# Performance work log

Hardware: AMD Instinct MI355X
Metric: run time of the kernel (lower is better)

Reference implementation:

```python
import jax, jax.numpy as jnp
import numpy as np

N = 4000                      # number of Gaussians
VOL = (256, 256, 256)         # volume shape
W = 32                        # fixed local window size (covers max 3-sigma box)
SIG_LO, SIG_HI = 0.008, 0.018 # normalized-coordinate sigma range


def setup_inputs() -> dict:
    key = jax.random.key(0)
    k1, k2, k3 = jax.random.split(key, 3)
    centers = jax.random.uniform(k1, (N, 3), dtype=jnp.float32)            # normalized in [0,1]
    sigmas = SIG_LO + (SIG_HI - SIG_LO) * jax.random.uniform(k2, (N,), dtype=jnp.float32)
    intensities = jax.random.uniform(k3, (N,), dtype=jnp.float32)
    return {"centers": centers, "sigmas": sigmas, "intensities": intensities}


def reference(centers, sigmas, intensities):
    shape = jnp.array(VOL, dtype=jnp.int32)                 # (3,)
    scale = (shape - 1).astype(jnp.float32)                 # volume_shape - 1, as in torch

    center = centers * scale                                # (N,3) voxel coords
    cutoff = 3.0 * sigmas[:, None] * scale                  # (N,3)

    # Bounding box: min_idx = int(max(center-cutoff, 0)), max (exclusive) = min(int(min(center+cutoff, scale))+1, dim)
    min_f = jnp.maximum(center - cutoff, 0.0)
    max_f = jnp.minimum(center + cutoff, scale)
    min_i = jnp.floor(min_f).astype(jnp.int32)              # (N,3) inclusive
    max_i = jnp.minimum(jnp.floor(max_f).astype(jnp.int32) + 1, shape)  # (N,3) exclusive

    # Fixed-size window fully inside the volume; mask voxels outside the true bbox.
    start = jnp.clip(min_i, 0, shape - W)                   # (N,3)
    offs = jnp.arange(W, dtype=jnp.int32)
    idx = start[:, :, None] + offs                          # (N,3,W) voxel indices per axis
    valid = (idx >= min_i[:, :, None]) & (idx < max_i[:, :, None])  # (N,3,W)

    # Per-axis squared distance in normalized coords (grid = idx/(dim-1)).
    pos = idx.astype(jnp.float32) / scale[None, :, None]    # (N,3,W)
    d2 = (pos - centers[:, :, None]) ** 2                   # (N,3,W)
    dist2 = (d2[:, 0, :, None, None] + d2[:, 1, None, :, None] + d2[:, 2, None, None, :])  # (N,W,W,W)

    inv2s2 = 0.5 / (sigmas ** 2)                            # (N,)
    contrib = intensities[:, None, None, None] * jnp.exp(-dist2 * inv2s2[:, None, None, None])
    mask = (valid[:, 0, :, None, None] & valid[:, 1, None, :, None] & valid[:, 2, None, None, :])
    contrib = jnp.where(mask, contrib, 0.0)                 # (N,W,W,W)

    # Overlapping scatter-add into the flattened volume.
    lin = (idx[:, 0, :, None, None] * (VOL[1] * VOL[2])
           + idx[:, 1, None, :, None] * VOL[2]
           + idx[:, 2, None, None, :])                      # (N,W,W,W) int32
    vol = jnp.zeros(VOL[0] * VOL[1] * VOL[2], dtype=jnp.float32)
    vol = vol.at[lin.reshape(-1)].add(contrib.reshape(-1))
    return vol.reshape(VOL)
```

## Files before the change

kernel.cpp:

```cpp
#include <hip/hip_runtime.h>

#define VOLD 256
#define CXD 16
#define CYD 16
#define CZD 32
#define NCELLS 2048
#define CAP 80

typedef float nfloat4 __attribute__((ext_vector_type(4)));
typedef float f2 __attribute__((ext_vector_type(2)));

__global__ __launch_bounds__(256) void splat_kernel(
    const float* __restrict__ centers, const float* __restrict__ sigmas,
    const float* __restrict__ intens, float* __restrict__ vol, int N)
{
    const int cell = blockIdx.x;
    const int czc = cell & 7;
    const int cyc = (cell >> 3) & 15;
    const int cxc = cell >> 7;
    const int vx0 = cxc * CXD, vy0 = cyc * CYD, vz0 = czc * CZD;
    const int t = threadIdx.x;

    __shared__ int           lcnt;
    __shared__ float4        pc4[CAP];
    __shared__ float         pint[CAP];
    __shared__ float         wx[CAP][CXD];
    __shared__ float         wy[CAP][CYD];
    __shared__ float         wz[CAP][CZD];
    __shared__ unsigned char wlist[4][CAP];

    if (t == 0) lcnt = 0;
    __syncthreads();

    const float axh = (float)(vx0 + CXD) + 0.5f, axl = (float)vx0 - 0.5f;
    const float ayh = (float)(vy0 + CYD) + 0.5f, ayl = (float)vy0 - 0.5f;
    const float azh = (float)(vz0 + CZD) + 0.5f, azl = (float)vz0 - 0.5f;

    const float4* c4 = (const float4*)centers;
    const float4* s4 = (const float4*)sigmas;
    const int npack = N >> 2;
    for (int i = t; i < npack; i += 256) {
        const float4 f0  = c4[3 * i];
        const float4 f1  = c4[3 * i + 1];
        const float4 f2v = c4[3 * i + 2];
        const float4 sg4 = s4[i];
        const float gx[4] = {f0.x, f0.w, f1.z, f2v.y};
        const float gy[4] = {f0.y, f1.x, f1.w, f2v.z};
        const float gz[4] = {f0.z, f1.y, f2v.x, f2v.w};
        const float gs[4] = {sg4.x, sg4.y, sg4.z, sg4.w};
        #pragma unroll
        for (int u = 0; u < 4; ++u) {
            const float m1 = fmaxf(fmaxf(fmaf(gx[u], 255.0f, -axh),
                                         fmaf(gy[u], 255.0f, -ayh)),
                                         fmaf(gz[u], 255.0f, -azh));
            const float m2 = fmaxf(fmaxf(fmaf(-gx[u], 255.0f, axl),
                                         fmaf(-gy[u], 255.0f, ayl)),
                                         fmaf(-gz[u], 255.0f, azl));
            if (fmaxf(m1, m2) < gs[u] * 765.0f) {
                const int p = atomicAdd(&lcnt, 1);
                if (p < CAP) {
                    pc4[p]  = make_float4(gx[u], gy[u], gz[u], gs[u]);
                    pint[p] = intens[4 * i + u];
                }
            }
        }
    }
    for (int g = (npack << 2) + t; g < N; g += 256) {
        const float cx = centers[3 * g], cy = centers[3 * g + 1], cz = centers[3 * g + 2];
        const float sg = sigmas[g];
        const float m1 = fmaxf(fmaxf(fmaf(cx, 255.0f, -axh), fmaf(cy, 255.0f, -ayh)),
                               fmaf(cz, 255.0f, -azh));
        const float m2 = fmaxf(fmaxf(fmaf(-cx, 255.0f, axl), fmaf(-cy, 255.0f, ayl)),
                               fmaf(-cz, 255.0f, azl));
        if (fmaxf(m1, m2) < sg * 765.0f) {
            const int p = atomicAdd(&lcnt, 1);
            if (p < CAP) { pc4[p] = make_float4(cx, cy, cz, sg); pint[p] = intens[g]; }
        }
    }
    __syncthreads();
    const int K = min(lcnt, CAP);

    for (int i = t; i < K * CXD; i += 256) {
        const int g = i >> 4, o = i & 15;
        const float4 p = pc4[g];
        const float cn = p.x, sig = p.w;
        const float cv = cn * 255.0f, cut = 3.0f * sig * 255.0f;
        const float fi = (float)(vx0 + o);
        float wv = 0.0f;
        if ((fi + 1.0f > cv - cut) && (fi <= fminf(cv + cut, 255.0f))) {
            const float d = fi * (1.0f / 255.0f) - cn;
            wv = __expf(-d * d * (0.5f / (sig * sig))) * pint[g];
        }
        wx[g][o] = wv;
    }
    for (int i = t; i < K * CYD; i += 256) {
        const int g = i >> 4, o = i & 15;
        const float4 p = pc4[g];
        const float cn = p.y, sig = p.w;
        const float cv = cn * 255.0f, cut = 3.0f * sig * 255.0f;
        const float fi = (float)(vy0 + o);
        float wv = 0.0f;
        if ((fi + 1.0f > cv - cut) && (fi <= fminf(cv + cut, 255.0f))) {
            const float d = fi * (1.0f / 255.0f) - cn;
            wv = __expf(-d * d * (0.5f / (sig * sig)));
        }
        wy[g][o] = wv;
    }
    for (int i = t; i < K * CZD; i += 256) {
        const int g = i >> 5, o = i & 31;
        const float4 p = pc4[g];
        const float cn = p.z, sig = p.w;
        const float cv = cn * 255.0f, cut = 3.0f * sig * 255.0f;
        const float fi = (float)(vz0 + o);
        float wv = 0.0f;
        if ((fi + 1.0f > cv - cut) && (fi <= fminf(cv + cut, 255.0f))) {
            const float d = fi * (1.0f / 255.0f) - cn;
            wv = __expf(-d * d * (0.5f / (sig * sig)));
        }
        wz[g][o] = wv;
    }
    __syncthreads();

    const int wv_id = t >> 6;
    const int lane  = t & 63;
    const float xw0 = (float)(vx0 + 8 * (wv_id & 1));
    const float yw0 = (float)(vy0 + 8 * (wv_id >> 1));

    int Kw = 0;
    for (int j0 = 0; j0 < K; j0 += 64) {
        const int j = j0 + lane;
        bool rel = false;
        if (j < K) {
            const float4 p = pc4[j];
            const float cvx = p.x * 255.0f, cvy = p.y * 255.0f;
            const float cut = p.w * 765.0f;
            rel = (cvx + cut >= xw0 - 1.0f) && (cvx - cut <= xw0 + 9.0f) &&
                  (cvy + cut >= yw0 - 1.0f) && (cvy - cut <= yw0 + 9.0f);
        }
        const unsigned long long m = __ballot(rel);
        if (rel) {
            const int pos = Kw + __popcll(m & ((1ull << lane) - 1ull));
            wlist[wv_id][pos] = (unsigned char)j;
        }
        Kw += __popcll(m);
    }

    const int zq = t & 7;
    const int xi = (t >> 3) & 15;
    const int yh = t >> 7;

    f2 acc[8][2];
    #pragma unroll
    for (int i = 0; i < 8; ++i) { acc[i][0] = 0.0f; acc[i][1] = 0.0f; }

    if (Kw > 0) {
        const unsigned char* wl = wlist[wv_id];
        const int kd0 = wl[0];
        const int kd1 = wl[(Kw > 1) ? 1 : 0];
        int kI2 = wl[(Kw > 2) ? 2 : (Kw - 1)];

        float4 ya0 = *(const float4*)&wy[kd0][8 * yh];
        float4 yb0 = *(const float4*)&wy[kd0][8 * yh + 4];
        float4 z0  = *(const float4*)&wz[kd0][4 * zq];
        float  x0v = wx[kd0][xi];
        float4 ya1 = *(const float4*)&wy[kd1][8 * yh];
        float4 yb1 = *(const float4*)&wy[kd1][8 * yh + 4];
        float4 z1  = *(const float4*)&wz[kd1][4 * zq];
        float  x1v = wx[kd1][xi];

        #pragma unroll 2
        for (int j = 0; j < Kw; ++j) {
            const int kI3 = wl[(j + 3 < Kw) ? (j + 3) : (Kw - 1)];
            const float4 ya2 = *(const float4*)&wy[kI2][8 * yh];
            const float4 yb2 = *(const float4*)&wy[kI2][8 * yh + 4];
            const float4 z2  = *(const float4*)&wz[kI2][4 * zq];
            const float  x2v = wx[kI2][xi];

            const f2 cz0 = {z0.x, z0.y};
            const f2 cz1 = {z0.z, z0.w};
            const float p0 = ya0.x * x0v, p1 = ya0.y * x0v;
            const float p2 = ya0.z * x0v, p3 = ya0.w * x0v;
            const float p4 = yb0.x * x0v, p5 = yb0.y * x0v;
            const float p6 = yb0.z * x0v, p7 = yb0.w * x0v;
            acc[0][0] += p0 * cz0; acc[0][1] += p0 * cz1;
            acc[1][0] += p1 * cz0; acc[1][1] += p1 * cz1;
            acc[2][0] += p2 * cz0; acc[2][1] += p2 * cz1;
            acc[3][0] += p3 * cz0; acc[3][1] += p3 * cz1;
            acc[4][0] += p4 * cz0; acc[4][1] += p4 * cz1;
            acc[5][0] += p5 * cz0; acc[5][1] += p5 * cz1;
            acc[6][0] += p6 * cz0; acc[6][1] += p6 * cz1;
            acc[7][0] += p7 * cz0; acc[7][1] += p7 * cz1;

            ya0 = ya1; yb0 = yb1; z0 = z1; x0v = x1v;
            ya1 = ya2; yb1 = yb2; z1 = z2; x1v = x2v;
            kI2 = kI3;
        }
    }

    #pragma unroll
    for (int yy = 0; yy < 8; ++yy) {
        const int y = 8 * yh + yy;
        const size_t lin = (size_t)(vx0 + xi) * (VOLD * VOLD)
                         + (size_t)(vy0 + y) * VOLD + (size_t)(vz0 + 4 * zq);
        nfloat4 v;
        v.x = acc[yy][0].x; v.y = acc[yy][0].y;
        v.z = acc[yy][1].x; v.w = acc[yy][1].y;
        __builtin_nontemporal_store(v, (nfloat4*)&vol[lin]);
    }
}

extern "C" void kernel_launch(void* const* d_in, const int* in_sizes, int n_in,
                              void* d_out, int out_size, void* d_ws, size_t ws_size,
                              hipStream_t stream) {
    const float* centers = (const float*)d_in[0];
    const float* sigmas  = (const float*)d_in[1];
    const float* intens  = (const float*)d_in[2];
    float* vol = (float*)d_out;
    const int N = in_sizes[1];

    splat_kernel<<<NCELLS, 256, 0, stream>>>(centers, sigmas, intens, vol, N);
}
```

Measured before the change: 25.57 us.

## Process two cells per block and replace syncthreads with lgkm-only barriers

Halves the grid to 1024 blocks, each looping over two cells (blockIdx and blockIdx+1024), with a per-cell counter so the shared counter needs no reset barrier. __syncthreads is replaced by a custom barrier that waits only on LDS/scalar counters, not global memory, so the nontemporal stores of the first cell need not drain before the second cell starts. The aim is to cut launch/tail overhead and overlap global stores with the next cell's culling. The cost is less parallelism across the GPU's CUs and serial per-block work.

```diff
diff --git a/kernel.cpp b/kernel.cpp
--- a/kernel.cpp
+++ b/kernel.cpp
@@ -4,24 +4,26 @@
 #define CXD 16
 #define CYD 16
 #define CZD 32
-#define NCELLS 2048
+#define NBLK 1024
 #define CAP 80
 
 typedef float nfloat4 __attribute__((ext_vector_type(4)));
 typedef float f2 __attribute__((ext_vector_type(2)));
+
+#define LGKM_BAR() do {                                     \
+    asm volatile("s_waitcnt lgkmcnt(0)" ::: "memory");      \
+    __builtin_amdgcn_sched_barrier(0);                      \
+    __builtin_amdgcn_s_barrier();                           \
+    __builtin_amdgcn_sched_barrier(0);                      \
+  } while (0)
 
 __global__ __launch_bounds__(256) void splat_kernel(
     const float* __restrict__ centers, const float* __restrict__ sigmas,
     const float* __restrict__ intens, float* __restrict__ vol, int N)
 {
-    const int cell = blockIdx.x;
-    const int czc = cell & 7;
-    const int cyc = (cell >> 3) & 15;
-    const int cxc = cell >> 7;
-    const int vx0 = cxc * CXD, vy0 = cyc * CYD, vz0 = czc * CZD;
     const int t = threadIdx.x;
 
-    __shared__ int           lcnt;
+    __shared__ int           lcnt[2];
     __shared__ float4        pc4[CAP];
     __shared__ float         pint[CAP];
     __shared__ float         wx[CAP][CXD];
@@ -29,183 +31,194 @@
     __shared__ float         wz[CAP][CZD];
     __shared__ unsigned char wlist[4][CAP];
 
-    if (t == 0) lcnt = 0;
-    __syncthreads();
-
-    const float axh = (float)(vx0 + CXD) + 0.5f, axl = (float)vx0 - 0.5f;
-    const float ayh = (float)(vy0 + CYD) + 0.5f, ayl = (float)vy0 - 0.5f;
-    const float azh = (float)(vz0 + CZD) + 0.5f, azl = (float)vz0 - 0.5f;
+    if (t < 2) lcnt[t] = 0;
 
     const float4* c4 = (const float4*)centers;
     const float4* s4 = (const float4*)sigmas;
     const int npack = N >> 2;
-    for (int i = t; i < npack; i += 256) {
-        const float4 f0  = c4[3 * i];
-        const float4 f1  = c4[3 * i + 1];
-        const float4 f2v = c4[3 * i + 2];
-        const float4 sg4 = s4[i];
-        const float gx[4] = {f0.x, f0.w, f1.z, f2v.y};
-        const float gy[4] = {f0.y, f1.x, f1.w, f2v.z};
-        const float gz[4] = {f0.z, f1.y, f2v.x, f2v.w};
-        const float gs[4] = {sg4.x, sg4.y, sg4.z, sg4.w};
+
+    #pragma unroll
+    for (int cc = 0; cc < 2; ++cc) {
+        const int cell = blockIdx.x + cc * NBLK;
+        const int czc = cell & 7;
+        const int cyc = (cell >> 3) & 15;
+        const int cxc = cell >> 7;
+        const int vx0 = cxc * CXD, vy0 = cyc * CYD, vz0 = czc * CZD;
+
+        LGKM_BAR();
+
+        const float axh = (float)(vx0 + CXD) + 0.5f, axl = (float)vx0 - 0.5f;
+        const float ayh = (float)(vy0 + CYD) + 0.5f, ayl = (float)vy0 - 0.5f;
+        const float azh = (float)(vz0 + CZD) + 0.5f, azl = (float)vz0 - 0.5f;
+
+        for (int i = t; i < npack; i += 256) {
+            const float4 f0  = c4[3 * i];
+            const float4 f1  = c4[3 * i + 1];
+            const float4 f2v = c4[3 * i + 2];
+            const float4 sg4 = s4[i];
+            const float gx[4] = {f0.x, f0.w, f1.z, f2v.y};
+            const float gy[4] = {f0.y, f1.x, f1.w, f2v.z};
+            const float gz[4] = {f0.z, f1.y, f2v.x, f2v.w};
+            const float gs[4] = {sg4.x, sg4.y, sg4.z, sg4.w};
+            #pragma unroll
+            for (int u = 0; u < 4; ++u) {
+                const float m1 = fmaxf(fmaxf(fmaf(gx[u], 255.0f, -axh),
+                                             fmaf(gy[u], 255.0f, -ayh)),
+                                             fmaf(gz[u], 255.0f, -azh));
+                const float m2 = fmaxf(fmaxf(fmaf(-gx[u], 255.0f, axl),
+                                             fmaf(-gy[u], 255.0f, ayl)),
+                                             fmaf(-gz[u], 255.0f, azl));
+                if (fmaxf(m1, m2) < gs[u] * 765.0f) {
+                    const int p = atomicAdd(&lcnt[cc], 1);
+                    if (p < CAP) {
+                        pc4[p]  = make_float4(gx[u], gy[u], gz[u], gs[u]);
+                        pint[p] = intens[4 * i + u];
+                    }
+                }
+            }
+        }
+        for (int g = (npack << 2) + t; g < N; g += 256) {
+            const float cx = centers[3 * g], cy = centers[3 * g + 1], cz = centers[3 * g + 2];
+            const float sg = sigmas[g];
+            const float m1 = fmaxf(fmaxf(fmaf(cx, 255.0f, -axh), fmaf(cy, 255.0f, -ayh)),
+                                   fmaf(cz, 255.0f, -azh));
+            const float m2 = fmaxf(fmaxf(fmaf(-cx, 255.0f, axl), fmaf(-cy, 255.0f, ayl)),
+                                   fmaf(-cz, 255.0f, azl));
+            if (fmaxf(m1, m2) < sg * 765.0f) {
+                const int p = atomicAdd(&lcnt[cc], 1);
+                if (p < CAP) { pc4[p] = make_float4(cx, cy, cz, sg); pint[p] = intens[g]; }
+            }
+        }
+        LGKM_BAR();
+        const int K = min(lcnt[cc], CAP);
+
+        for (int i = t; i < K * CXD; i += 256) {
+            const int g = i >> 4, o = i & 15;
+            const float4 p = pc4[g];
+            const float cn = p.x, sig = p.w;
+            const float cv = cn * 255.0f, cut = 3.0f * sig * 255.0f;
+            const float fi = (float)(vx0 + o);
+            float wv = 0.0f;
+            if ((fi + 1.0f > cv - cut) && (fi <= fminf(cv + cut, 255.0f))) {
+                const float d = fi * (1.0f / 255.0f) - cn;
+                wv = __expf(-d * d * (0.5f / (sig * sig))) * pint[g];
+            }
+            wx[g][o] = wv;
+        }
+        for (int i = t; i < K * CYD; i += 256) {
+            const int g = i >> 4, o = i & 15;
+            const float4 p = pc4[g];
+            const float cn = p.y, sig = p.w;
+            const float cv = cn * 255.0f, cut = 3.0f * sig * 255.0f;
+            const float fi = (float)(vy0 + o);
+            float wv = 0.0f;
+            if ((fi + 1.0f > cv - cut) && (fi <= fminf(cv + cut, 255.0f))) {
+                const float d = fi * (1.0f / 255.0f) - cn;
+                wv = __expf(-d * d * (0.5f / (sig * sig)));
+            }
+            wy[g][o] = wv;
+        }
+        for (int i = t; i < K * CZD; i += 256) {
+            const int g = i >> 5, o = i & 31;
+            const float4 p = pc4[g];
+            const float cn = p.z, sig = p.w;
+            const float cv = cn * 255.0f, cut = 3.0f * sig * 255.0f;
+            const float fi = (float)(vz0 + o);
+            float wv = 0.0f;
+            if ((fi + 1.0f > cv - cut) && (fi <= fminf(cv + cut, 255.0f))) {
+                const float d = fi * (1.0f / 255.0f) - cn;
+                wv = __expf(-d * d * (0.5f / (sig * sig)));
+            }
+            wz[g][o] = wv;
+        }
+        LGKM_BAR();
+
+        const int wv_id = t >> 6;
+        const int lane  = t & 63;
+        const float xw0 = (float)(vx0 + 8 * (wv_id & 1));
+        const float yw0 = (float)(vy0 + 8 * (wv_id >> 1));
+
+        int Kw = 0;
+        for (int j0 = 0; j0 < K; j0 += 64) {
+            const int j = j0 + lane;
+            bool rel = false;
+            if (j < K) {
+                const float4 p = pc4[j];
+                const float cvx = p.x * 255.0f, cvy = p.y * 255.0f;
+                const float cut = p.w * 765.0f;
+                rel = (cvx + cut >= xw0 - 1.0f) && (cvx - cut <= xw0 + 9.0f) &&
+                      (cvy + cut >= yw0 - 1.0f) && (cvy - cut <= yw0 + 9.0f);
+            }
+            const unsigned long long m = __ballot(rel);
+            if (rel) {
+                const int pos = Kw + __popcll(m & ((1ull << lane) - 1ull));
+                wlist[wv_id][pos] = (unsigned char)j;
+            }
+            Kw += __popcll(m);
+        }
+
+        const int zq = t & 7;
+        const int xi = (t >> 3) & 15;
+        const int yh = t >> 7;
+
+        f2 acc[8][2];
         #pragma unroll
-        for (int u = 0; u < 4; ++u) {
-            const float m1 = fmaxf(fmaxf(fmaf(gx[u], 255.0f, -axh),
-                                         fmaf(gy[u], 255.0f, -ayh)),
-                                         fmaf(gz[u], 255.0f, -azh));
-            const float m2 = fmaxf(fmaxf(fmaf(-gx[u], 255.0f, axl),
-                                         fmaf(-gy[u], 255.0f, ayl)),
-                                         fmaf(-gz[u], 255.0f, azl));
-            if (fmaxf(m1, m2) < gs[u] * 765.0f) {
-                const int p = atomicAdd(&lcnt, 1);
-                if (p < CAP) {
-                    pc4[p]  = make_float4(gx[u], gy[u], gz[u], gs[u]);
-                    pint[p] = intens[4 * i + u];
-                }
-            }
-        }
-    }
-    for (int g = (npack << 2) + t; g < N; g += 256) {
-        const float cx = centers[3 * g], cy = centers[3 * g + 1], cz = centers[3 * g + 2];
-        const float sg = sigmas[g];
-        const float m1 = fmaxf(fmaxf(fmaf(cx, 255.0f, -axh), fmaf(cy, 255.0f, -ayh)),
-                               fmaf(cz, 255.0f, -azh));
-        const float m2 = fmaxf(fmaxf(fmaf(-cx, 255.0f, axl), fmaf(-cy, 255.0f, ayl)),
-                               fmaf(-cz, 255.0f, azl));
-        if (fmaxf(m1, m2) < sg * 765.0f) {
-            const int p = atomicAdd(&lcnt, 1);
-            if (p < CAP) { pc4[p] = make_float4(cx, cy, cz, sg); pint[p] = intens[g]; }
-        }
-    }
-    __syncthreads();
-    const int K = min(lcnt, CAP);
-
-    for (int i = t; i < K * CXD; i += 256) {
-        const int g = i >> 4, o = i & 15;
-        const float4 p = pc4[g];
-        const float cn = p.x, sig = p.w;
-        const float cv = cn * 255.0f, cut = 3.0f * sig * 255.0f;
-        const float fi = (float)(vx0 + o);
-        float wv = 0.0f;
-        if ((fi + 1.0f > cv - cut) && (fi <= fminf(cv + cut, 255.0f))) {
-            const float d = fi * (1.0f / 255.0f) - cn;
-            wv = __expf(-d * d * (0.5f / (sig * sig))) * pint[g];
-        }
-        wx[g][o] = wv;
-    }
-    for (int i = t; i < K * CYD; i += 256) {
-        const int g = i >> 4, o = i & 15;
-        const float4 p = pc4[g];
-        const float cn = p.y, sig = p.w;
-        const float cv = cn * 255.0f, cut = 3.0f * sig * 255.0f;
-        const float fi = (float)(vy0 + o);
-        float wv = 0.0f;
-        if ((fi + 1.0f > cv - cut) && (fi <= fminf(cv + cut, 255.0f))) {
-            const float d = fi * (1.0f / 255.0f) - cn;
-            wv = __expf(-d * d * (0.5f / (sig * sig)));
-        }
-        wy[g][o] = wv;
-    }
-    for (int i = t; i < K * CZD; i += 256) {
-        const int g = i >> 5, o = i & 31;
-        const float4 p = pc4[g];
-        const float cn = p.z, sig = p.w;
-        const float cv = cn * 255.0f, cut = 3.0f * sig * 255.0f;
-        const float fi = (float)(vz0 + o);
-        float wv = 0.0f;
-        if ((fi + 1.0f > cv - cut) && (fi <= fminf(cv + cut, 255.0f))) {
-            const float d = fi * (1.0f / 255.0f) - cn;
-            wv = __expf(-d * d * (0.5f / (sig * sig)));
-        }
-        wz[g][o] = wv;
-    }
-    __syncthreads();
-
-    const int wv_id = t >> 6;
-    const int lane  = t & 63;
-    const float xw0 = (float)(vx0 + 8 * (wv_id & 1));
-    const float yw0 = (float)(vy0 + 8 * (wv_id >> 1));
-
-    int Kw = 0;
-    for (int j0 = 0; j0 < K; j0 += 64) {
-        const int j = j0 + lane;
-        bool rel = false;
-        if (j < K) {
-            const float4 p = pc4[j];
-            const float cvx = p.x * 255.0f, cvy = p.y * 255.0f;
-            const float cut = p.w * 765.0f;
-            rel = (cvx + cut >= xw0 - 1.0f) && (cvx - cut <= xw0 + 9.0f) &&
-                  (cvy + cut >= yw0 - 1.0f) && (cvy - cut <= yw0 + 9.0f);
-        }
-        const unsigned long long m = __ballot(rel);
-        if (rel) {
-            const int pos = Kw + __popcll(m & ((1ull << lane) - 1ull));
-            wlist[wv_id][pos] = (unsigned char)j;
-        }
-        Kw += __popcll(m);
-    }
-
-    const int zq = t & 7;
-    const int xi = (t >> 3) & 15;
-    const int yh = t >> 7;
-
-    f2 acc[8][2];
-    #pragma unroll
-    for (int i = 0; i < 8; ++i) { acc[i][0] = 0.0f; acc[i][1] = 0.0f; }
-
-    if (Kw > 0) {
-        const unsigned char* wl = wlist[wv_id];
-        const int kd0 = wl[0];
-        const int kd1 = wl[(Kw > 1) ? 1 : 0];
-        int kI2 = wl[(Kw > 2) ? 2 : (Kw - 1)];
-
-        float4 ya0 = *(const float4*)&wy[kd0][8 * yh];
-        float4 yb0 = *(const float4*)&wy[kd0][8 * yh + 4];
-        float4 z0  = *(const float4*)&wz[kd0][4 * zq];
-        float  x0v = wx[kd0][xi];
-        float4 ya1 = *(const float4*)&wy[kd1][8 * yh];
-        float4 yb1 = *(const float4*)&wy[kd1][8 * yh + 4];
-        float4 z1  = *(const float4*)&wz[kd1][4 * zq];
-        float  x1v = wx[kd1][xi];
-
-        #pragma unroll 2
-        for (int j = 0; j < Kw; ++j) {
-            const int kI3 = wl[(j + 3 < Kw) ? (j + 3) : (Kw - 1)];
-            const float4 ya2 = *(const float4*)&wy[kI2][8 * yh];
-            const float4 yb2 = *(const float4*)&wy[kI2][8 * yh + 4];
-            const float4 z2  = *(const float4*)&wz[kI2][4 * zq];
-            const float  x2v = wx[kI2][xi];
-
-            const f2 cz0 = {z0.x, z0.y};
-            const f2 cz1 = {z0.z, z0.w};
-            const float p0 = ya0.x * x0v, p1 = ya0.y * x0v;
-            const float p2 = ya0.z * x0v, p3 = ya0.w * x0v;
-            const float p4 = yb0.x * x0v, p5 = yb0.y * x0v;
-            const float p6 = yb0.z * x0v, p7 = yb0.w * x0v;
-            acc[0][0] += p0 * cz0; acc[0][1] += p0 * cz1;
-            acc[1][0] += p1 * cz0; acc[1][1] += p1 * cz1;
-            acc[2][0] += p2 * cz0; acc[2][1] += p2 * cz1;
-            acc[3][0] += p3 * cz0; acc[3][1] += p3 * cz1;
-            acc[4][0] += p4 * cz0; acc[4][1] += p4 * cz1;
-            acc[5][0] += p5 * cz0; acc[5][1] += p5 * cz1;
-            acc[6][0] += p6 * cz0; acc[6][1] += p6 * cz1;
-            acc[7][0] += p7 * cz0; acc[7][1] += p7 * cz1;
-
-            ya0 = ya1; yb0 = yb1; z0 = z1; x0v = x1v;
-            ya1 = ya2; yb1 = yb2; z1 = z2; x1v = x2v;
-            kI2 = kI3;
-        }
-    }
-
-    #pragma unroll
-    for (int yy = 0; yy < 8; ++yy) {
-        const int y = 8 * yh + yy;
-        const size_t lin = (size_t)(vx0 + xi) * (VOLD * VOLD)
-                         + (size_t)(vy0 + y) * VOLD + (size_t)(vz0 + 4 * zq);
-        nfloat4 v;
-        v.x = acc[yy][0].x; v.y = acc[yy][0].y;
-        v.z = acc[yy][1].x; v.w = acc[yy][1].y;
-        __builtin_nontemporal_store(v, (nfloat4*)&vol[lin]);
+        for (int i = 0; i < 8; ++i) { acc[i][0] = 0.0f; acc[i][1] = 0.0f; }
+
+        if (Kw > 0) {
+            const unsigned char* wl = wlist[wv_id];
+            const int kd0 = wl[0];
+            const int kd1 = wl[(Kw > 1) ? 1 : 0];
+            int kI2 = wl[(Kw > 2) ? 2 : (Kw - 1)];
+
+            float4 ya0 = *(const float4*)&wy[kd0][8 * yh];
+            float4 yb0 = *(const float4*)&wy[kd0][8 * yh + 4];
+            float4 z0  = *(const float4*)&wz[kd0][4 * zq];
+            float  x0v = wx[kd0][xi];
+            float4 ya1 = *(const float4*)&wy[kd1][8 * yh];
+            float4 yb1 = *(const float4*)&wy[kd1][8 * yh + 4];
+            float4 z1  = *(const float4*)&wz[kd1][4 * zq];
+            float  x1v = wx[kd1][xi];
+
+            #pragma unroll 2
+            for (int j = 0; j < Kw; ++j) {
+                const int kI3 = wl[(j + 3 < Kw) ? (j + 3) : (Kw - 1)];
+                const float4 ya2 = *(const float4*)&wy[kI2][8 * yh];
+                const float4 yb2 = *(const float4*)&wy[kI2][8 * yh + 4];
+                const float4 z2  = *(const float4*)&wz[kI2][4 * zq];
+                const float  x2v = wx[kI2][xi];
+
+                const f2 cz0 = {z0.x, z0.y};
+                const f2 cz1 = {z0.z, z0.w};
+                const float p0 = ya0.x * x0v, p1 = ya0.y * x0v;
+                const float p2 = ya0.z * x0v, p3 = ya0.w * x0v;
+                const float p4 = yb0.x * x0v, p5 = yb0.y * x0v;
+                const float p6 = yb0.z * x0v, p7 = yb0.w * x0v;
+                acc[0][0] += p0 * cz0; acc[0][1] += p0 * cz1;
+                acc[1][0] += p1 * cz0; acc[1][1] += p1 * cz1;
+                acc[2][0] += p2 * cz0; acc[2][1] += p2 * cz1;
+                acc[3][0] += p3 * cz0; acc[3][1] += p3 * cz1;
+                acc[4][0] += p4 * cz0; acc[4][1] += p4 * cz1;
+                acc[5][0] += p5 * cz0; acc[5][1] += p5 * cz1;
+                acc[6][0] += p6 * cz0; acc[6][1] += p6 * cz1;
+                acc[7][0] += p7 * cz0; acc[7][1] += p7 * cz1;
+
+                ya0 = ya1; yb0 = yb1; z0 = z1; x0v = x1v;
+                ya1 = ya2; yb1 = yb2; z1 = z2; x1v = x2v;
+                kI2 = kI3;
+            }
+        }
+
+        #pragma unroll
+        for (int yy = 0; yy < 8; ++yy) {
+            const int y = 8 * yh + yy;
+            const size_t lin = (size_t)(vx0 + xi) * (VOLD * VOLD)
+                             + (size_t)(vy0 + y) * VOLD + (size_t)(vz0 + 4 * zq);
+            nfloat4 v;
+            v.x = acc[yy][0].x; v.y = acc[yy][0].y;
+            v.z = acc[yy][1].x; v.w = acc[yy][1].y;
+            __builtin_nontemporal_store(v, (nfloat4*)&vol[lin]);
+        }
     }
 }
 
@@ -218,5 +231,5 @@
     float* vol = (float*)d_out;
     const int N = in_sizes[1];
 
-    splat_kernel<<<NCELLS, 256, 0, stream>>>(centers, sigmas, intens, vol, N);
+    splat_kernel<<<NBLK, 256, 0, stream>>>(centers, sigmas, intens, vol, N);
 }
```

Result: no change. 25.57 us (-0.0%).
